# Kernel tuning notes

Measured on AMD Instinct MI355X. Metric: run time of the kernel, lower is better.

The kernel has to match this reference:

```python
import jax, jax.numpy as jnp
from jax import lax
import numpy as np

B, N, WID = 4096, 16, 64


def setup_inputs() -> dict:
    key = jax.random.key(0)
    ks = jax.random.split(key, 10)
    def nrm(k, shape, fan):
        return (jax.random.normal(k, shape) / np.float32(np.sqrt(fan))).astype(jnp.float32)
    x = 2.0 * jax.random.randint(ks[0], (B, N, N), 0, 2).astype(jnp.float32) - 1.0  # spins +/-1
    return {
        "x": x,
        "Wx": nrm(ks[1], (1, 2), 2),          # intermediate_x: Linear(2,1,bias=False)
        "Wh": nrm(ks[2], (WID, 2 * WID), 2 * WID),   # intermediate_h
        "Wh2": nrm(ks[3], (WID, 2 * WID), 2 * WID),  # intermediate_h2
        "Wih": nrm(ks[4], (4 * WID, 2), 2),   # LSTMCell weight_ih
        "Whh": nrm(ks[5], (4 * WID, WID), WID),  # LSTMCell weight_hh
        "bih": nrm(ks[6], (4 * WID,), WID),
        "bhh": nrm(ks[7], (4 * WID,), WID),
        "Wfc": nrm(ks[8], (2, WID), WID),     # fc1
        "bfc": nrm(ks[9], (2,), WID),
    }


def _log_prob(x, Wx, Wh, Wh2, Wih, Whh, bih, bhh, Wfc, bfc):
    Bn, n, _ = x.shape
    Wd = Whh.shape[1]
    dt = x.dtype

    # zigzag traversal: even rows left->right, odd rows right->left.
    # perm maps traversal position t -> column index; involutive (identity or reversal).
    perms = jnp.stack([jnp.arange(n) if i % 2 == 0 else jnp.arange(n)[::-1]
                       for i in range(n)])  # [n, n]
    x_rows = jnp.transpose(x, (1, 0, 2))                                  # [n, B, n]
    x_up_rows = jnp.concatenate([jnp.zeros((1, Bn, n), dt), x_rows[:-1]], 0)  # [n, B, n]

    Wh_p, Wh_u = Wh[:, :Wd], Wh[:, Wd:]
    Wh2_p, Wh2_u = Wh2[:, :Wd], Wh2[:, Wd:]

    def cell(carry, xs):
        h_prev, c_prev = carry          # [B, W] each (in-row previous cell, zeros at row start)
        x_prev, x_up, h_up, c_up = xs   # [B], [B], [B,W], [B,W]
        # slot 1 = previous cell along traversal, slot 2 = cell above
        x_inter = x_prev * Wx[0, 0] + x_up * Wx[0, 1]                     # [B]
        h_inter = h_prev @ Wh_p.T + h_up @ Wh_u.T                          # [B, W]
        c_inter = c_prev @ Wh2_p.T + c_up @ Wh2_u.T                        # [B, W]
        xh = (x_inter + 1.0) * 0.5
        emb = jnp.stack([xh, 1.0 - xh], axis=-1)                           # [B, 2]
        gates = emb @ Wih.T + bih + h_inter @ Whh.T + bhh                  # [B, 4W]
        ig, fg, gg, og = jnp.split(gates, 4, axis=-1)
        c_new = jax.nn.sigmoid(fg) * c_inter + jax.nn.sigmoid(ig) * jnp.tanh(gg)
        h_new = jax.nn.sigmoid(og) * jnp.tanh(c_new)
        y = jax.nn.log_softmax(h_new @ Wfc.T + bfc, axis=-1)               # [B, 2]
        return (h_new, c_new), (h_new, c_new, y)

    def row_step(carry, xs):
        h_row, c_row = carry            # [B, n, W] states of previous row (column order)
        x_row, x_up_row, perm = xs
        x_trav = x_row[:, perm]                                            # [B, n]
        x_prev_trav = jnp.concatenate([jnp.zeros((Bn, 1), dt), x_trav[:, :-1]], 1)
        x_up_trav = x_up_row[:, perm]
        h_up_trav = jnp.transpose(h_row[:, perm], (1, 0, 2))               # [n, B, W]
        c_up_trav = jnp.transpose(c_row[:, perm], (1, 0, 2))
        init = (jnp.zeros((Bn, Wd), dt), jnp.zeros((Bn, Wd), dt))
        _, (h_t, c_t, y_t) = lax.scan(
            cell, init, (x_prev_trav.T, x_up_trav.T, h_up_trav, c_up_trav))
        # traversal order -> column order (perm is its own inverse)
        h_col = jnp.transpose(h_t[perm], (1, 0, 2))                        # [B, n, W]
        c_col = jnp.transpose(c_t[perm], (1, 0, 2))
        y_col = y_t[perm]                                                  # [n, B, 2]
        return (h_col, c_col), y_col

    init = (jnp.zeros((Bn, n, Wd), dt), jnp.zeros((Bn, n, Wd), dt))
    _, ys = lax.scan(row_step, init, (x_rows, x_up_rows, perms))           # [n, n, B, 2]
    y = jnp.transpose(ys, (2, 0, 1, 3))                                    # [B, n, n, 2]

    mask = (1.0 + x) * 0.5
    lp = y[..., 0] * mask + y[..., 1] * (1.0 - mask)                       # [B, n, n]
    # final correction: samples with exactly one up spin
    aa = mask.sum((1, 2))
    rec = aa == 1
    jc = 0 if n % 2 == 0 else n - 1  # last visited cell of the zigzag
    factor = jnp.where(rec, 1.0 - mask[:, n - 1, jc], jnp.ones((), dt))
    lp = lp.at[:, n - 1, jc].multiply(factor)
    return lp.sum((1, 2))


def reference(x, Wx, Wh, Wh2, Wih, Whh, bih, bhh, Wfc, bfc):
    return _log_prob(x, Wx, Wh, Wh2, Wih, Whh, bih, bhh, Wfc, bfc)
```

## Files before the change

kernel.cpp:

```cpp
#include <hip/hip_runtime.h>

typedef __bf16 bf16x8 __attribute__((ext_vector_type(8)));
typedef float f32x4 __attribute__((ext_vector_type(4)));

#define MFMA(a,b,c) __builtin_amdgcn_mfma_f32_16x16x32_bf16((a),(b),(c),0,0,0)

__device__ __forceinline__ float rcp_(float x){ return __builtin_amdgcn_rcpf(x); }

#define L2E 1.4426950408889634f
#define LN2 0.6931471805599453f

__global__ __launch_bounds__(256) void prep_kernel(
    const float* __restrict__ Wh,  const float* __restrict__ Wh2,
    const float* __restrict__ Whh, const float* __restrict__ Wfc,
    const float* __restrict__ Wih, const float* __restrict__ bih,
    const float* __restrict__ bhh,
    char* __restrict__ tblc)
{
  const int idx = blockIdx.x*256 + threadIdx.x;
  if (idx < 512*14*8){
    const int e = idx & 7, f = (idx >> 3) % 14, t = (idx >> 3) / 14;
    const int w = t >> 6, lane = t & 63, l16 = lane & 15;
    const int g8 = ((lane >> 4) & 3) * 8;
    const int hcol = w*8 + (l16 & 7), hi = l16 >> 3;
    float val;
    if (f < 8){
      const int half = (f >> 2) & 1;
      const int tile = (f >> 1) & 1;
      const int s    = f & 1;
      const int gate = tile*2 + hi;
      const int n = gate*64 + hcol;
      const int k = s*32 + g8 + e;
      float acc = 0.f;
      for (int j=0; j<64; ++j) acc += Whh[n*64 + j] * Wh[j*128 + half*64 + k];
      val = acc * ((gate == 2) ? 2.f*L2E : L2E);
    } else if (f < 12){
      const int s = f - 8;
      const int k = (s & 1)*32 + g8 + e;
      val = Wh2[hcol*128 + (s >> 1)*64 + k];
    } else {
      const int k = (f & 1)*32 + g8 + e;
      val = Wfc[k] - Wfc[64 + k];
    }
    *(__bf16*)(tblc + t*240 + f*16 + e*2) = (__bf16)val;
  } else if (idx < 512*14*8 + 512*4){
    const int j = idx - 512*14*8;
    const int t = j >> 2, q = j & 3;
    const int w = t >> 6, lane = t & 63, l16 = lane & 15, hi = l16 >> 3;
    const int tile = q >> 1, kind = q & 1;
    const int gate = tile*2 + hi;
    const int n = gate*64 + w*8 + (l16 & 7);
    const float sc = (gate == 2) ? 2.f*L2E : L2E;
    const float v = kind ? sc*(Wih[n*2] - Wih[n*2+1])
                         : sc*(bih[n] + bhh[n] + Wih[n*2+1]);
    *(float*)(tblc + t*240 + 224 + q*4) = v;
  }
}

__global__ __launch_bounds__(512,2) void lstm2d_kernel(
    const float* __restrict__ x,   const float* __restrict__ Wx,
    const float* __restrict__ bfc,
    const char* __restrict__ tblc,
    float* __restrict__ out)
{
  __shared__ __align__(16) __bf16 s_h[16*16*64];
  __shared__ __align__(16) __bf16 s_c[16*16*64];
  __shared__ __align__(16) float  s_xh[256*16];
  __shared__ __align__(16) float  s_d[256*16];
  __shared__ unsigned int s_msk[16*8];
  __shared__ float s_red[8*16];

  const int tid  = threadIdx.x;
  const int w    = tid >> 6;
  const int lane = tid & 63;
  const int l16  = lane & 15;
  const int g4   = lane >> 4;
  const int g8   = g4 * 8;
  const int hi   = l16 >> 3;
  const bool lo  = (hi == 0);

  const float wx0 = Wx[0], wx1 = Wx[1];
  const float bd  = bfc[0] - bfc[1];

  unsigned int* zh = (unsigned int*)s_h;
  unsigned int* zc = (unsigned int*)s_c;
  #pragma unroll
  for (int it=0; it<16; ++it){ zh[tid + it*512] = 0u; zc[tid + it*512] = 0u; }

  const float* xg = x + blockIdx.x * 4096;
  #pragma unroll
  for (int k=0; k<8; ++k){
    const int idx = tid + k*512;
    const int row = idx & 15, slot = idx >> 4;
    const int i = slot >> 4, t = slot & 15;
    const int c   = (i & 1) ? 15 - t : t;
    const int cpc = (i & 1) ? c + 1 : c - 1;
    const float xp = (t > 0) ? xg[row*256 + i*16 + cpc] : 0.f;
    const float xu = (i > 0) ? xg[row*256 + (i-1)*16 + c] : 0.f;
    s_xh[slot*16 + row] = (xp*wx0 + xu*wx1 + 1.f) * 0.5f;
  }
  if (tid < 128){
    const int row = tid >> 3, wd = tid & 7;
    unsigned int m = 0;
    for (int b=0; b<32; ++b){
      const int slot = wd*32 + b, i = slot >> 4, t = slot & 15;
      const int c = (i & 1) ? 15 - t : t;
      if (xg[row*256 + i*16 + c] > 0.f) m |= (1u << b);
    }
    s_msk[row*8 + wd] = m;
  }

  const char* tb = tblc + tid*240;
  bf16x8 g1T0[2], g1T1[2], g2T0[2], g2T1[2], cB[4], fcB[2];
  g1T0[0] = *(const bf16x8*)(tb +   0); g1T0[1] = *(const bf16x8*)(tb +  16);
  g1T1[0] = *(const bf16x8*)(tb +  32); g1T1[1] = *(const bf16x8*)(tb +  48);
  g2T0[0] = *(const bf16x8*)(tb +  64); g2T0[1] = *(const bf16x8*)(tb +  80);
  g2T1[0] = *(const bf16x8*)(tb +  96); g2T1[1] = *(const bf16x8*)(tb + 112);
  #pragma unroll
  for (int s=0; s<4; ++s) cB[s] = *(const bf16x8*)(tb + 128 + s*16);
  fcB[0] = *(const bf16x8*)(tb + 192); fcB[1] = *(const bf16x8*)(tb + 208);
  const float base0 = *(const float*)(tb + 224);
  const float dvec0 = *(const float*)(tb + 228);
  const float base1 = *(const float*)(tb + 232);
  const float dvec1 = *(const float*)(tb + 236);

  const int offA0 = l16*64 + ((     g8) ^ ((l16 & 7) << 3));
  const int offA1 = l16*64 + ((32 + g8) ^ ((l16 & 7) << 3));
  const int habs = w*8 + (l16 & 7);
  int stWa[2];
  #pragma unroll
  for (int e=0; e<2; ++e){
    const int R = g4*4 + 2*hi + e;
    stWa[e] = R*64 + (habs ^ ((R & 7) << 3));
  }
  const float C2 = -2.f*L2E;

  __syncthreads();

  f32x4 aT0u, aT1u, aCu;

  for (int i=0; i<16; ++i){
    const int dir = i & 1;
    const int slot0 = i*16;

    {
      const int bu = (dir ? 15 : 0) << 10;
      bf16x8 h0 = *(const bf16x8*)(s_h + bu + offA0);
      bf16x8 h1 = *(const bf16x8*)(s_h + bu + offA1);
      bf16x8 c0 = *(const bf16x8*)(s_c + bu + offA0);
      bf16x8 c1 = *(const bf16x8*)(s_c + bu + offA1);
      const float4 xh4 = *(const float4*)(s_xh + slot0*16 + g4*4);
      #pragma unroll
      for (int r=0;r<4;++r){
        const float xh = (&xh4.x)[r];
        aT0u[r] = base0 + xh*dvec0;
        aT1u[r] = base1 + xh*dvec1;
      }
      aT0u = MFMA(h0, g2T0[0], aT0u); aT0u = MFMA(h1, g2T0[1], aT0u);
      aT1u = MFMA(h0, g2T1[0], aT1u); aT1u = MFMA(h1, g2T1[1], aT1u);
      f32x4 z = {0.f,0.f,0.f,0.f};
      aCu = MFMA(c0, cB[2], z); aCu = MFMA(c1, cB[3], aCu);
      if (w == 0 && i > 0){
        f32x4 fz = {bd,bd,bd,bd};
        fz = MFMA(h0, fcB[0], fz);
        f32x4 aF = MFMA(h1, fcB[1], fz);
        if (l16 == 0){
          #pragma unroll
          for (int r=0;r<4;++r) s_d[(slot0-1)*16 + g4*4 + r] = aF[r];
        }
      }
    }

    for (int t=0; t<16; ++t){
      const int c    = dir ? 15 - t : t;
      const int slot = slot0 + t;

      f32x4 aT0 = aT0u, aT1 = aT1u, aC = aCu;
      if (t > 0){
        const int bp = (dir ? c + 1 : c - 1) << 10;
        bf16x8 a0 = *(const bf16x8*)(s_h + bp + offA0);
        bf16x8 a1 = *(const bf16x8*)(s_h + bp + offA1);
        bf16x8 q0 = *(const bf16x8*)(s_c + bp + offA0);
        bf16x8 q1 = *(const bf16x8*)(s_c + bp + offA1);
        aT0 = MFMA(a0, g1T0[0], aT0); aT0 = MFMA(a1, g1T0[1], aT0);
        aT1 = MFMA(a0, g1T1[0], aT1); aT1 = MFMA(a1, g1T1[1], aT1);
        aC  = MFMA(q0, cB[0], aC);    aC  = MFMA(q1, cB[1], aC);
        if (w == 0){
          f32x4 fz = {bd,bd,bd,bd};
          fz = MFMA(a0, fcB[0], fz);
          f32x4 aF = MFMA(a1, fcB[1], fz);
          if (l16 == 0){
            #pragma unroll
            for (int r=0;r<4;++r) s_d[(slot-1)*16 + g4*4 + r] = aF[r];
          }
        }
      }

      if (t < 15){
        const int bu = (dir ? 14 - t : t + 1) << 10;
        bf16x8 h0 = *(const bf16x8*)(s_h + bu + offA0);
        bf16x8 h1 = *(const bf16x8*)(s_h + bu + offA1);
        bf16x8 c0 = *(const bf16x8*)(s_c + bu + offA0);
        bf16x8 c1 = *(const bf16x8*)(s_c + bu + offA1);
        const float4 xh4 = *(const float4*)(s_xh + (slot+1)*16 + g4*4);
        #pragma unroll
        for (int r=0;r<4;++r){
          const float xh = (&xh4.x)[r];
          aT0u[r] = base0 + xh*dvec0;
          aT1u[r] = base1 + xh*dvec1;
        }
        aT0u = MFMA(h0, g2T0[0], aT0u); aT0u = MFMA(h1, g2T0[1], aT0u);
        aT1u = MFMA(h0, g2T1[0], aT1u); aT1u = MFMA(h1, g2T1[1], aT1u);
        f32x4 z = {0.f,0.f,0.f,0.f};
        aCu = MFMA(c0, cB[2], z); aCu = MFMA(c1, cB[3], aCu);
      }

      const int cb = c << 10;
      #pragma unroll
      for (int e=0; e<2; ++e){
        const float sendT0 = lo ? aT0[2+e] : aT0[e];
        const float sendT1 = lo ? aT1[2+e] : aT1[e];
        const float rT0 = __shfl_xor(sendT0, 8);
        const float rT1 = __shfl_xor(sendT1, 8);
        const float own0 = lo ? aT0[e] : aT0[2+e];
        const float own1 = lo ? aT1[e] : aT1[2+e];
        const float ig = lo ? own0 : rT0;
        const float fg = lo ? rT0  : own0;
        const float gg = lo ? own1 : rT1;
        const float og = lo ? rT1  : own1;
        const float cI = lo ? aC[e] : aC[2+e];
        const float si = rcp_(1.f + exp2f(-ig));
        const float sf = rcp_(1.f + exp2f(-fg));
        const float tg = 2.f * rcp_(1.f + exp2f(-gg)) - 1.f;
        const float cn = sf*cI + si*tg;
        const float so = rcp_(1.f + exp2f(-og));
        const float tc = 2.f * rcp_(1.f + exp2f(C2*cn)) - 1.f;
        const float hn = so * tc;
        s_h[cb + stWa[e]] = (__bf16)hn;
        s_c[cb + stWa[e]] = (__bf16)cn;
      }

      __syncthreads();
    }
  }

  if (w == 0){
    bf16x8 a0 = *(const bf16x8*)(s_h + offA0);
    bf16x8 a1 = *(const bf16x8*)(s_h + offA1);
    f32x4 fz = {bd,bd,bd,bd};
    fz = MFMA(a0, fcB[0], fz);
    f32x4 aF = MFMA(a1, fcB[1], fz);
    if (l16 == 0){
      #pragma unroll
      for (int r=0;r<4;++r) s_d[255*16 + g4*4 + r] = aF[r];
    }
  }
  __syncthreads();

  {
    const int row = tid & 15, grp = tid >> 4;
    float lpp = 0.f;
    #pragma unroll
    for (int e=0; e<8; ++e){
      const int slot = grp*8 + e;
      const float d = s_d[slot*16 + row];
      const int msk = (s_msk[row*8 + (slot >> 5)] >> (slot & 31)) & 1;
      const float zz = msk ? -d : d;
      lpp -= LN2 * log2f(1.f + exp2f(zz * L2E));
    }
    lpp += __shfl_xor(lpp, 16);
    lpp += __shfl_xor(lpp, 32);
    if (lane < 16) s_red[w*16 + lane] = lpp;
  }
  __syncthreads();
  if (tid < 16){
    const int row = tid;
    float lp = 0.f;
    #pragma unroll
    for (int ww=0; ww<8; ++ww) lp += s_red[ww*16 + row];
    int aa = 0;
    #pragma unroll
    for (int wd=0; wd<8; ++wd) aa += __popc(s_msk[row*8 + wd]);
    const int m255 = (s_msk[row*8 + 7] >> 31) & 1;
    if (aa == 1 && m255){
      const float d = s_d[255*16 + row];
      lp += LN2 * log2f(1.f + exp2f(-d * L2E));
    }
    out[blockIdx.x*16 + row] = lp;
  }
}

extern "C" void kernel_launch(void* const* d_in, const int* in_sizes, int n_in,
                              void* d_out, int out_size, void* d_ws, size_t ws_size,
                              hipStream_t stream) {
  const float* x   = (const float*)d_in[0];
  const float* Wx  = (const float*)d_in[1];
  const float* Wh  = (const float*)d_in[2];
  const float* Wh2 = (const float*)d_in[3];
  const float* Wih = (const float*)d_in[4];
  const float* Whh = (const float*)d_in[5];
  const float* bih = (const float*)d_in[6];
  const float* bhh = (const float*)d_in[7];
  const float* Wfc = (const float*)d_in[8];
  const float* bfc = (const float*)d_in[9];
  float* out = (float*)d_out;
  char* tbl = (char*)d_ws;

  prep_kernel<<<dim3(((512*14*8 + 512*4) + 255)/256), dim3(256), 0, stream>>>(
      Wh, Wh2, Whh, Wfc, Wih, bih, bhh, tbl);
  lstm2d_kernel<<<dim3(256), dim3(512), 0, stream>>>(x, Wx, bfc, tbl, out);
}
```

Baseline: 274.4 us.

## Halve batch rows per block to launch 512 blocks and spread fc work

Each block now handles 8 batch samples instead of 16, so the grid doubles to 512 blocks and fills more of the GPU's compute units; LDS buffers shrink and launch bounds allow 4 blocks per SM. The 16-row MFMA tiles are now half padding (rows duplicated, only g4<2 lanes write results), which wastes MFMA throughput. The fc1 projection is rotated across waves instead of always running on wave 0, to balance per-step work. Total MFMA and sync work per sample roughly doubles in exchange for more parallelism on a latency-bound recurrence.

Result: slower. 439.0 us (+60.0%).

```diff
diff --git a/kernel.cpp b/kernel.cpp
--- a/kernel.cpp
+++ b/kernel.cpp
@@ -57,18 +57,18 @@
   }
 }
 
-__global__ __launch_bounds__(512,2) void lstm2d_kernel(
+__global__ __launch_bounds__(512,4) void lstm2d_kernel(
     const float* __restrict__ x,   const float* __restrict__ Wx,
     const float* __restrict__ bfc,
     const char* __restrict__ tblc,
     float* __restrict__ out)
 {
-  __shared__ __align__(16) __bf16 s_h[16*16*64];
-  __shared__ __align__(16) __bf16 s_c[16*16*64];
-  __shared__ __align__(16) float  s_xh[256*16];
-  __shared__ __align__(16) float  s_d[256*16];
-  __shared__ unsigned int s_msk[16*8];
-  __shared__ float s_red[8*16];
+  __shared__ __align__(16) __bf16 s_h[16*8*64];
+  __shared__ __align__(16) __bf16 s_c[16*8*64];
+  __shared__ __align__(16) float  s_xh[256*8];
+  __shared__ __align__(16) float  s_d[256*8];
+  __shared__ unsigned int s_msk[8*8];
+  __shared__ float s_red[64];
 
   const int tid  = threadIdx.x;
   const int w    = tid >> 6;
@@ -78,6 +78,8 @@
   const int g8   = g4 * 8;
   const int hi   = l16 >> 3;
   const bool lo  = (hi == 0);
+  const int rl   = l16 & 7;
+  const bool vld = (g4 < 2);
 
   const float wx0 = Wx[0], wx1 = Wx[1];
   const float bd  = bfc[0] - bfc[1];
@@ -85,21 +87,21 @@
   unsigned int* zh = (unsigned int*)s_h;
   unsigned int* zc = (unsigned int*)s_c;
   #pragma unroll
-  for (int it=0; it<16; ++it){ zh[tid + it*512] = 0u; zc[tid + it*512] = 0u; }
-
-  const float* xg = x + blockIdx.x * 4096;
+  for (int it=0; it<8; ++it){ zh[tid + it*512] = 0u; zc[tid + it*512] = 0u; }
+
+  const float* xg = x + blockIdx.x * 2048;
   #pragma unroll
-  for (int k=0; k<8; ++k){
+  for (int k=0; k<4; ++k){
     const int idx = tid + k*512;
-    const int row = idx & 15, slot = idx >> 4;
+    const int row = idx & 7, slot = idx >> 3;
     const int i = slot >> 4, t = slot & 15;
     const int c   = (i & 1) ? 15 - t : t;
     const int cpc = (i & 1) ? c + 1 : c - 1;
     const float xp = (t > 0) ? xg[row*256 + i*16 + cpc] : 0.f;
     const float xu = (i > 0) ? xg[row*256 + (i-1)*16 + c] : 0.f;
-    s_xh[slot*16 + row] = (xp*wx0 + xu*wx1 + 1.f) * 0.5f;
-  }
-  if (tid < 128){
+    s_xh[slot*8 + row] = (xp*wx0 + xu*wx1 + 1.f) * 0.5f;
+  }
+  if (tid < 64){
     const int row = tid >> 3, wd = tid & 7;
     unsigned int m = 0;
     for (int b=0; b<32; ++b){
@@ -124,15 +126,16 @@
   const float base1 = *(const float*)(tb + 232);
   const float dvec1 = *(const float*)(tb + 236);
 
-  const int offA0 = l16*64 + ((     g8) ^ ((l16 & 7) << 3));
-  const int offA1 = l16*64 + ((32 + g8) ^ ((l16 & 7) << 3));
+  const int offA0 = rl*64 + ((     g8) ^ (rl << 3));
+  const int offA1 = rl*64 + ((32 + g8) ^ (rl << 3));
   const int habs = w*8 + (l16 & 7);
   int stWa[2];
   #pragma unroll
   for (int e=0; e<2; ++e){
-    const int R = g4*4 + 2*hi + e;
-    stWa[e] = R*64 + (habs ^ ((R & 7) << 3));
-  }
+    const int R = (g4 & 1)*4 + 2*hi + e;
+    stWa[e] = R*64 + (habs ^ (R << 3));
+  }
+  const int xhOff = (g4 & 1) * 4;
   const float C2 = -2.f*L2E;
 
   __syncthreads();
@@ -144,12 +147,12 @@
     const int slot0 = i*16;
 
     {
-      const int bu = (dir ? 15 : 0) << 10;
+      const int bu = (dir ? 15 : 0) << 9;
       bf16x8 h0 = *(const bf16x8*)(s_h + bu + offA0);
       bf16x8 h1 = *(const bf16x8*)(s_h + bu + offA1);
       bf16x8 c0 = *(const bf16x8*)(s_c + bu + offA0);
       bf16x8 c1 = *(const bf16x8*)(s_c + bu + offA1);
-      const float4 xh4 = *(const float4*)(s_xh + slot0*16 + g4*4);
+      const float4 xh4 = *(const float4*)(s_xh + slot0*8 + xhOff);
       #pragma unroll
       for (int r=0;r<4;++r){
         const float xh = (&xh4.x)[r];
@@ -160,13 +163,13 @@
       aT1u = MFMA(h0, g2T1[0], aT1u); aT1u = MFMA(h1, g2T1[1], aT1u);
       f32x4 z = {0.f,0.f,0.f,0.f};
       aCu = MFMA(c0, cB[2], z); aCu = MFMA(c1, cB[3], aCu);
-      if (w == 0 && i > 0){
+      if (i > 0 && w == 7){
         f32x4 fz = {bd,bd,bd,bd};
         fz = MFMA(h0, fcB[0], fz);
         f32x4 aF = MFMA(h1, fcB[1], fz);
-        if (l16 == 0){
+        if (l16 == 0 && vld){
           #pragma unroll
-          for (int r=0;r<4;++r) s_d[(slot0-1)*16 + g4*4 + r] = aF[r];
+          for (int r=0;r<4;++r) s_d[(slot0-1)*8 + (g4&1)*4 + r] = aF[r];
         }
       }
     }
@@ -177,7 +180,7 @@
 
       f32x4 aT0 = aT0u, aT1 = aT1u, aC = aCu;
       if (t > 0){
-        const int bp = (dir ? c + 1 : c - 1) << 10;
+        const int bp = (dir ? c + 1 : c - 1) << 9;
         bf16x8 a0 = *(const bf16x8*)(s_h + bp + offA0);
         bf16x8 a1 = *(const bf16x8*)(s_h + bp + offA1);
         bf16x8 q0 = *(const bf16x8*)(s_c + bp + offA0);
@@ -185,24 +188,24 @@
         aT0 = MFMA(a0, g1T0[0], aT0); aT0 = MFMA(a1, g1T0[1], aT0);
         aT1 = MFMA(a0, g1T1[0], aT1); aT1 = MFMA(a1, g1T1[1], aT1);
         aC  = MFMA(q0, cB[0], aC);    aC  = MFMA(q1, cB[1], aC);
-        if (w == 0){
+        if (w == ((t - 1) & 7)){
           f32x4 fz = {bd,bd,bd,bd};
           fz = MFMA(a0, fcB[0], fz);
           f32x4 aF = MFMA(a1, fcB[1], fz);
-          if (l16 == 0){
+          if (l16 == 0 && vld){
             #pragma unroll
-            for (int r=0;r<4;++r) s_d[(slot-1)*16 + g4*4 + r] = aF[r];
+            for (int r=0;r<4;++r) s_d[(slot-1)*8 + (g4&1)*4 + r] = aF[r];
           }
         }
       }
 
       if (t < 15){
-        const int bu = (dir ? 14 - t : t + 1) << 10;
+        const int bu = (dir ? 14 - t : t + 1) << 9;
         bf16x8 h0 = *(const bf16x8*)(s_h + bu + offA0);
         bf16x8 h1 = *(const bf16x8*)(s_h + bu + offA1);
         bf16x8 c0 = *(const bf16x8*)(s_c + bu + offA0);
         bf16x8 c1 = *(const bf16x8*)(s_c + bu + offA1);
-        const float4 xh4 = *(const float4*)(s_xh + (slot+1)*16 + g4*4);
+        const float4 xh4 = *(const float4*)(s_xh + (slot+1)*8 + xhOff);
         #pragma unroll
         for (int r=0;r<4;++r){
           const float xh = (&xh4.x)[r];
@@ -215,78 +218,82 @@
         aCu = MFMA(c0, cB[2], z); aCu = MFMA(c1, cB[3], aCu);
       }
 
-      const int cb = c << 10;
-      #pragma unroll
-      for (int e=0; e<2; ++e){
-        const float sendT0 = lo ? aT0[2+e] : aT0[e];
-        const float sendT1 = lo ? aT1[2+e] : aT1[e];
-        const float rT0 = __shfl_xor(sendT0, 8);
-        const float rT1 = __shfl_xor(sendT1, 8);
-        const float own0 = lo ? aT0[e] : aT0[2+e];
-        const float own1 = lo ? aT1[e] : aT1[2+e];
-        const float ig = lo ? own0 : rT0;
-        const float fg = lo ? rT0  : own0;
-        const float gg = lo ? own1 : rT1;
-        const float og = lo ? rT1  : own1;
-        const float cI = lo ? aC[e] : aC[2+e];
-        const float si = rcp_(1.f + exp2f(-ig));
-        const float sf = rcp_(1.f + exp2f(-fg));
-        const float tg = 2.f * rcp_(1.f + exp2f(-gg)) - 1.f;
-        const float cn = sf*cI + si*tg;
-        const float so = rcp_(1.f + exp2f(-og));
-        const float tc = 2.f * rcp_(1.f + exp2f(C2*cn)) - 1.f;
-        const float hn = so * tc;
-        s_h[cb + stWa[e]] = (__bf16)hn;
-        s_c[cb + stWa[e]] = (__bf16)cn;
+      if (vld){
+        const int cb = c << 9;
+        #pragma unroll
+        for (int e=0; e<2; ++e){
+          const float sendT0 = lo ? aT0[2+e] : aT0[e];
+          const float sendT1 = lo ? aT1[2+e] : aT1[e];
+          const float rT0 = __shfl_xor(sendT0, 8);
+          const float rT1 = __shfl_xor(sendT1, 8);
+          const float own0 = lo ? aT0[e] : aT0[2+e];
+          const float own1 = lo ? aT1[e] : aT1[2+e];
+          const float ig = lo ? own0 : rT0;
+          const float fg = lo ? rT0  : own0;
+          const float gg = lo ? own1 : rT1;
+          const float og = lo ? rT1  : own1;
+          const float cI = lo ? aC[e] : aC[2+e];
+          const float si = rcp_(1.f + exp2f(-ig));
+          const float sf = rcp_(1.f + exp2f(-fg));
+          const float tg = 2.f * rcp_(1.f + exp2f(-gg)) - 1.f;
+          const float cn = sf*cI + si*tg;
+          const float so = rcp_(1.f + exp2f(-og));
+          const float tc = 2.f * rcp_(1.f + exp2f(C2*cn)) - 1.f;
+          const float hn = so * tc;
+          s_h[cb + stWa[e]] = (__bf16)hn;
+          s_c[cb + stWa[e]] = (__bf16)cn;
+        }
       }
 
       __syncthreads();
     }
   }
 
-  if (w == 0){
+  if (w == 7){
     bf16x8 a0 = *(const bf16x8*)(s_h + offA0);
     bf16x8 a1 = *(const bf16x8*)(s_h + offA1);
     f32x4 fz = {bd,bd,bd,bd};
     fz = MFMA(a0, fcB[0], fz);
     f32x4 aF = MFMA(a1, fcB[1], fz);
-    if (l16 == 0){
+    if (l16 == 0 && vld){
       #pragma unroll
-      for (int r=0;r<4;++r) s_d[255*16 + g4*4 + r] = aF[r];
+      for (int r=0;r<4;++r) s_d[255*8 + (g4&1)*4 + r] = aF[r];
     }
   }
   __syncthreads();
 
   {
-    const int row = tid & 15, grp = tid >> 4;
+    const int row = lane & 7, sub = lane >> 3;
+    const int grp = w*8 + sub;
     float lpp = 0.f;
     #pragma unroll
-    for (int e=0; e<8; ++e){
-      const int slot = grp*8 + e;
-      const float d = s_d[slot*16 + row];
+    for (int e=0; e<4; ++e){
+      const int slot = grp*4 + e;
+      const float d = s_d[slot*8 + row];
       const int msk = (s_msk[row*8 + (slot >> 5)] >> (slot & 31)) & 1;
       const float zz = msk ? -d : d;
       lpp -= LN2 * log2f(1.f + exp2f(zz * L2E));
     }
+    lpp += __shfl_xor(lpp, 8);
     lpp += __shfl_xor(lpp, 16);
     lpp += __shfl_xor(lpp, 32);
-    if (lane < 16) s_red[w*16 + lane] = lpp;
+    if (lane < 8) s_red[w*8 + lane] = lpp;
   }
   __syncthreads();
-  if (tid < 16){
+  if (tid < 8){
     const int row = tid;
     float lp = 0.f;
     #pragma unroll
-    for (int ww=0; ww<8; ++ww) lp += s_red[ww*16 + row];
+    for (int ww=0; ww<8; ++ww) lp += s_red[ww*8 + row];
     int aa = 0;
     #pragma unroll
     for (int wd=0; wd<8; ++wd) aa += __popc(s_msk[row*8 + wd]);
     const int m255 = (s_msk[row*8 + 7] >> 31) & 1;
     if (aa == 1 && m255){
-      const float d = s_d[255*16 + row];
+      const float d = s_d[255*8 + row];
       lp += LN2 * log2f(1.f + exp2f(-d * L2E));
     }
-    out[blockIdx.x*16 + row] = lp;
+    out[blockIdx.x*8 + row] = lp;
   }
 }
 
@@ -308,5 +315,5 @@
 
   prep_kernel<<<dim3(((512*14*8 + 512*4) + 255)/256), dim3(256), 0, stream>>>(
       Wh, Wh2, Whh, Wfc, Wih, bih, bhh, tbl);
-  lstm2d_kernel<<<dim3(256), dim3(512), 0, stream>>>(x, Wx, bfc, tbl, out);
+  lstm2d_kernel<<<dim3(512), dim3(512), 0, stream>>>(x, Wx, bfc, tbl, out);
 }
```
